# Kernel optimization log

Measured on AMD Instinct MI355X. Metric: run time of the kernel, lower is better.

## Reference

```python
import jax, jax.numpy as jnp
import numpy as np

N = 131072   # total nodes (B*C)
D = 128      # hidden_dim
H = 4        # gat_heads == hgt_heads
HD = 32      # head dim
T = 3        # number of edge types
E = 262144   # edges per edge type
B = 512      # graphs
EPS = 1e-6
SLOPE = 0.2  # LeakyReLU negative slope (module-wide and GAT internal)


def _rmsnorm(x, scale):
    return scale * x * jax.lax.rsqrt(jnp.mean(x * x, axis=-1, keepdims=True) + EPS)


def _gat(x, ei, W, a_src, a_dst, b):
    """HeteroConv(sum) of per-edge-type GATConv (concat heads, self-loops)."""
    loops = jnp.arange(N)

    def one(ei_t, W_t, as_t, ad_t):
        h = (x @ W_t).reshape(N, H, HD)                         # [N,H,HD]
        src = jnp.concatenate([ei_t[0], loops])                 # add self loops
        dst = jnp.concatenate([ei_t[1], loops])
        a = jax.nn.leaky_relu((h * as_t).sum(-1)[src] + (h * ad_t).sum(-1)[dst], SLOPE)  # [E',H]
        m = jax.ops.segment_max(a, dst, num_segments=N)
        ex = jnp.exp(a - m[dst])
        s = jax.ops.segment_sum(ex, dst, num_segments=N)
        alpha = ex / s[dst]                                     # segment softmax per dst
        out = jax.ops.segment_sum(h[src] * alpha[..., None], dst, num_segments=N)
        return out.reshape(N, D)

    return jax.vmap(one)(ei, W, a_src, a_dst).sum(0) + b.sum(0)


def _hgt(x, ei, kw, kb, qw, qb, vw, vb, rel_k, rel_v, rel_p, aw, ab, skip):
    """HGTConv, single node type, T edge types; softmax over all incoming edges."""
    k = (x @ kw + kb).reshape(N, H, HD)
    q = (x @ qw + qb).reshape(N, H, HD)
    v = (x @ vw + vb).reshape(N, H, HD)
    kt = jnp.einsum('nhd,thde->tnhe', k, rel_k)                 # relation-specific keys
    vt = jnp.einsum('nhd,thde->tnhe', v, rel_v)
    k_msg = jax.vmap(lambda a, i: a[i])(kt, ei[:, 0]).reshape(T * E, H, HD)
    v_msg = jax.vmap(lambda a, i: a[i])(vt, ei[:, 0]).reshape(T * E, H, HD)
    dst = ei[:, 1].reshape(T * E)
    p = jnp.broadcast_to(rel_p[:, None, :], (T, E, H)).reshape(T * E, H)
    score = (q[dst] * k_msg).sum(-1) * p / np.sqrt(HD)          # [T*E,H]
    m = jax.ops.segment_max(score, dst, num_segments=N)
    ex = jnp.exp(score - m[dst])
    s = jax.ops.segment_sum(ex, dst, num_segments=N)
    alpha = ex / s[dst]
    out = jax.ops.segment_sum(alpha[..., None] * v_msg, dst, num_segments=N).reshape(N, D)
    out = jax.nn.gelu(out, approximate=False) @ aw + ab
    g = jax.nn.sigmoid(skip)
    return g * out + (1.0 - g) * x


def _res(x_old, x_new, scale):
    # norm -> (dropout is identity in eval) -> residual -> LeakyReLU(0.2)
    return jax.nn.leaky_relu(x_old + _rmsnorm(x_new, scale), SLOPE)


def setup_inputs() -> dict:
    key = jax.random.key(0)
    ks = iter(jax.random.split(key, 48))

    def nrm(shape, std=0.1):
        return jax.random.normal(next(ks), shape, jnp.float32) * std

    inp = {}
    inp['x_cell'] = nrm((N, D), 1.0)
    inp['x_cell_embedded'] = nrm((N, D), 1.0)
    inp['z_h'] = nrm((B, D), 1.0)
    inp['edge_index'] = jax.random.randint(next(ks), (T, 2, E), 0, N)
    for l in ('gat1', 'gat2'):
        inp[l + '_w'] = nrm((T, D, H * HD))
        inp[l + '_att_src'] = nrm((T, H, HD))
        inp[l + '_att_dst'] = nrm((T, H, HD))
        inp[l + '_b'] = jnp.zeros((T, D), jnp.float32)
    inp['norm1_s'] = jnp.ones((D,), jnp.float32)
    inp['norm2_s'] = jnp.ones((D,), jnp.float32)
    inp['norm3_s'] = jnp.ones((D,), jnp.float32)
    for nm in ('k', 'q', 'v'):
        inp['hgt_%s_w' % nm] = nrm((D, D))
        inp['hgt_%s_b' % nm] = jnp.zeros((D,), jnp.float32)
    inp['hgt_rel_k'] = nrm((T, H, HD, HD))
    inp['hgt_rel_v'] = nrm((T, H, HD, HD))
    inp['hgt_rel_p'] = jnp.ones((T, H), jnp.float32)
    inp['hgt_a_w'] = nrm((D, D))
    inp['hgt_a_b'] = jnp.zeros((D,), jnp.float32)
    inp['hgt_skip'] = jnp.ones((), jnp.float32)
    inp['inj_w'] = nrm((D, D))
    inp['inj_b'] = jnp.zeros((D,), jnp.float32)
    inp['film_w1'] = nrm((D, 2 * D))
    inp['film_b1'] = jnp.zeros((2 * D,), jnp.float32)
    inp['film_w2'] = nrm((2 * D, 2 * D), 0.001)
    inp['film_b2'] = jnp.zeros((2 * D,), jnp.float32)
    inp['batch_size'] = B
    return inp


def reference(x_cell, x_cell_embedded, z_h, edge_index,
              gat1_w, gat1_att_src, gat1_att_dst, gat1_b,
              gat2_w, gat2_att_src, gat2_att_dst, gat2_b,
              norm1_s, norm2_s, norm3_s,
              hgt_k_w, hgt_k_b, hgt_q_w, hgt_q_b, hgt_v_w, hgt_v_b,
              hgt_rel_k, hgt_rel_v, hgt_rel_p, hgt_a_w, hgt_a_b, hgt_skip,
              inj_w, inj_b, film_w1, film_b1, film_w2, film_b2, batch_size):
    x1 = _res(x_cell, _gat(x_cell, edge_index, gat1_w, gat1_att_src, gat1_att_dst, gat1_b), norm1_s)
    x2 = _res(x1, _gat(x1, edge_index, gat2_w, gat2_att_src, gat2_att_dst, gat2_b), norm2_s)
    x3 = _res(x2, _hgt(x2, edge_index, hgt_k_w, hgt_k_b, hgt_q_w, hgt_q_b, hgt_v_w, hgt_v_b,
                       hgt_rel_k, hgt_rel_v, hgt_rel_p, hgt_a_w, hgt_a_b, hgt_skip), norm3_s)
    x3 = x3 + x_cell_embedded @ inj_w + inj_b                   # input injection
    # FiLM (per-graph z, fixed batch mode)
    gb = jax.nn.gelu(z_h @ film_w1 + film_b1, approximate=False) @ film_w2 + film_b2
    gamma, beta = jnp.split(gb, 2, axis=-1)
    gamma = 0.1 * jnp.tanh(gamma)
    beta = 0.1 * jnp.tanh(beta)
    C = N // batch_size
    out = (1.0 + gamma)[:, None, :] * x3.reshape(batch_size, C, D) + beta[:, None, :]
    return out.reshape(N, D)
```

## Files before the change

### kernel.cpp

```cpp
#include <hip/hip_runtime.h>
#include <math.h>
#include <cstdint>

#define NN     131072
#define DDIM   128
#define NHEAD  4
#define HDIM   32
#define NTYPE  3
#define NEDGE  262144
#define NGRAPH 512
#define EPSV   1e-6f
#define SLOPEV 0.2f

typedef unsigned short bfraw;
typedef __attribute__((ext_vector_type(8))) short bf16x8;
typedef __attribute__((ext_vector_type(4))) float f32x4;

__device__ __forceinline__ float lrelu(float x){ return x >= 0.f ? x : SLOPEV*x; }
__device__ __forceinline__ float gelu_f(float x){ return 0.5f*x*(1.f+erff(x*0.70710678118654752f)); }
__device__ __forceinline__ bfraw f2bf(float f){
  unsigned int u = __float_as_uint(f);
  u += 0x7fffu + ((u >> 16) & 1u);
  return (bfraw)(u >> 16);
}
__device__ __forceinline__ float4 ld_bf4(const bfraw* p){
  uint2 u = *reinterpret_cast<const uint2*>(p);
  float4 r;
  r.x = __uint_as_float(u.x << 16); r.y = __uint_as_float(u.x & 0xffff0000u);
  r.z = __uint_as_float(u.y << 16); r.w = __uint_as_float(u.y & 0xffff0000u);
  return r;
}
__device__ __forceinline__ bf16x8 pack_bf8(const float* p){
  float4 u = *reinterpret_cast<const float4*>(p);
  float4 v = *reinterpret_cast<const float4*>(p+4);
  bf16x8 r;
  r[0]=(short)f2bf(u.x); r[1]=(short)f2bf(u.y); r[2]=(short)f2bf(u.z); r[3]=(short)f2bf(u.w);
  r[4]=(short)f2bf(v.x); r[5]=(short)f2bf(v.y); r[6]=(short)f2bf(v.z); r[7]=(short)f2bf(v.w);
  return r;
}

__global__ void fill_k(float* __restrict__ p, float v, int n){
  int i = blockIdx.x*blockDim.x + threadIdx.x;
  int stride = gridDim.x*blockDim.x;
  for (; i < n; i += stride) p[i] = v;
}

__global__ void hist_k(const int* __restrict__ ei, int* __restrict__ deg){
  int idx = blockIdx.x*256 + threadIdx.x;
  int t = idx >> 18, e = idx & (NEDGE-1);
  int d = ei[(long)t*2*NEDGE + NEDGE + e];
  atomicAdd(&deg[t*NN + d], 1);
}

__global__ void scan_a_k(const int* __restrict__ deg, int* __restrict__ rp,
                         int* __restrict__ csum){
  __shared__ int sh[256];
  int t = blockIdx.y, chunk = blockIdx.x, tid = threadIdx.x;
  const int* dp = deg + (long)t*NN + chunk*2048 + tid*8;
  int v[8]; int s = 0;
  #pragma unroll
  for (int i=0;i<8;i++){ v[i] = dp[i]; s += v[i]; }
  sh[tid] = s; __syncthreads();
  for (int off=1; off<256; off<<=1){
    int x = (tid>=off) ? sh[tid-off] : 0;
    __syncthreads();
    sh[tid] += x;
    __syncthreads();
  }
  int run = sh[tid] - s;
  int* op = rp + (long)t*(NN+1) + chunk*2048 + tid*8;
  #pragma unroll
  for (int i=0;i<8;i++){ op[i] = run; run += v[i]; }
  if (tid == 255) csum[t*64 + chunk] = sh[255];
}

__global__ void scan_b_k(int* __restrict__ csum){
  __shared__ int sh[64];
  int t = blockIdx.x, tid = threadIdx.x;
  int s = csum[t*64 + tid];
  sh[tid] = s; __syncthreads();
  for (int off=1; off<64; off<<=1){
    int x = (tid>=off) ? sh[tid-off] : 0;
    __syncthreads();
    sh[tid] += x;
    __syncthreads();
  }
  csum[t*64 + tid] = sh[tid] - s;
}

__global__ void scan_c_k(int* __restrict__ rp, const int* __restrict__ csum){
  int t = blockIdx.y, chunk = blockIdx.x, tid = threadIdx.x;
  int add = csum[t*64 + chunk];
  int* op = rp + (long)t*(NN+1) + chunk*2048 + tid*8;
  #pragma unroll
  for (int i=0;i<8;i++) op[i] += add;
  if (chunk == 63 && tid == 255) rp[(long)t*(NN+1) + NN] = NEDGE;
}

__global__ void scatter_k(const int* __restrict__ ei, const int* __restrict__ rp,
                          int* __restrict__ cnt, int* __restrict__ srcs){
  int idx = blockIdx.x*256 + threadIdx.x;
  int t = idx >> 18, e = idx & (NEDGE-1);
  int s = ei[(long)t*2*NEDGE + e];
  int d = ei[(long)t*2*NEDGE + NEDGE + e];
  int pos = rp[(long)t*(NN+1) + d] + atomicAdd(&cnt[t*NN + d], 1);
  srcs[(long)t*NEDGE + pos] = s;
}

__global__ void wswz_k(const float* g0a, const float* g0b, const float* g0c,
                       const float* g1a, const float* g1b, const float* g1c,
                       const float* qw,
                       const float* wk, const float* wv,
                       const float* aw, const float* injw,
                       bfraw* __restrict__ Wall)
{
  int y = blockIdx.y;
  const float* src;
  switch(y){
    case 0: src = g0a; break;  case 1: src = g0b; break;  case 2: src = g0c; break;
    case 3: src = g1a; break;  case 4: src = g1b; break;  case 5: src = g1c; break;
    case 6: src = qw; break;
    case 7: case 8: case 9: src = wk + (long)(y-7)*16384; break;
    case 10: case 11: case 12: src = wv + (long)(y-10)*16384; break;
    case 13: src = aw; break;
    default: src = injw; break;
  }
  int i = blockIdx.x*256 + threadIdx.x;
  int j = i & 7, lane = (i>>3) & 63, kc = (i>>9) & 3, nt = i >> 11;
  int k = kc*32 + ((lane>>4)<<3) + j;
  int n = nt*16 + (lane & 15);
  Wall[(long)y*16384 + i] = f2bf(src[k*DDIM + n]);
}

__global__ void gatproj_k(const float* __restrict__ w, const float* __restrict__ asrc,
                          const float* __restrict__ adst, bfraw* __restrict__ out)
{
  int i = blockIdx.x*256 + threadIdx.x;
  int j = i & 7, lane = (i>>3) & 63, kc = (i>>9) & 3, nt = i >> 11;
  int k = kc*32 + ((lane>>4)<<3) + j;
  int n = nt*16 + (lane & 15);
  float s = 0.f;
  if (n < 24){
    int t = n >> 3, sd = (n >> 2) & 1, hh = n & 3;
    const float* a  = (sd ? adst : asrc) + ((long)t*NHEAD + hh)*HDIM;
    const float* wr = w + ((long)t*DDIM + k)*DDIM + hh*HDIM;
    #pragma unroll 8
    for (int dd=0; dd<HDIM; dd++) s += wr[dd]*a[dd];
  }
  out[i] = f2bf(s);
}

__device__ __forceinline__ void load_afrags_bf16(const bfraw* __restrict__ A,
    long blockRow, int tid, bf16x8 a0[4], bf16x8 a1[4])
{
  const int w = tid >> 6, lane = tid & 63;
  const long rowA = blockRow + w*32 + (lane & 15);
  const bfraw* A0 = A + rowA*DDIM + ((lane>>4)<<3);
  #pragma unroll
  for (int kc=0;kc<4;kc++){
    a0[kc] = *reinterpret_cast<const bf16x8*>(A0 + kc*32);
    a1[kc] = *reinterpret_cast<const bf16x8*>(A0 + 16*DDIM + kc*32);
  }
}

__device__ __forceinline__ void load_afrags_f32(const float* __restrict__ A,
    long blockRow, int tid, bf16x8 a0[4], bf16x8 a1[4])
{
  const int w = tid >> 6, lane = tid & 63;
  const long rowA = blockRow + w*32 + (lane & 15);
  const float* A0 = A + rowA*DDIM + ((lane>>4)<<3);
  #pragma unroll
  for (int kc=0;kc<4;kc++){
    a0[kc] = pack_bf8(A0 + kc*32);
    a1[kc] = pack_bf8(A0 + 16*DDIM + kc*32);
  }
}

__device__ __forceinline__ void mfma_128(const bfraw* Wl, int lane,
    bf16x8 a0[4], bf16x8 a1[4], f32x4 acc0[8], f32x4 acc1[8])
{
  const f32x4 zz = {0.f,0.f,0.f,0.f};
  #pragma unroll
  for (int nt=0;nt<8;nt++){ acc0[nt]=zz; acc1[nt]=zz; }
  #pragma unroll
  for (int nt=0;nt<8;nt++){
    #pragma unroll
    for (int kc=0;kc<4;kc++){
      bf16x8 b = *reinterpret_cast<const bf16x8*>(Wl + ((nt*4+kc)*64 + lane)*8);
      acc0[nt] = __builtin_amdgcn_mfma_f32_16x16x32_bf16(a0[kc], b, acc0[nt], 0, 0, 0);
      acc1[nt] = __builtin_amdgcn_mfma_f32_16x16x32_bf16(a1[kc], b, acc1[nt], 0, 0, 0);
    }
  }
}

__device__ __forceinline__ void gemm_store_bf16(f32x4 acc0[8], f32x4 acc1[8],
    const float* bias, bfraw* __restrict__ Cb, long blockRow, int tid)
{
  const int w = tid>>6, lane = tid&63, q = lane>>4;
  #pragma unroll
  for (int g=0; g<2; g++){
    #pragma unroll
    for (int nt=0;nt<8;nt++){
      int col = nt*16 + (lane & 15);
      float bv = bias ? bias[col] : 0.f;
      #pragma unroll
      for (int r=0;r<4;r++){
        long row = blockRow + w*32 + g*16 + q*4 + r;
        float v = (g ? acc1[nt][r] : acc0[nt][r]) + bv;
        Cb[row*DDIM + col] = f2bf(v);
      }
    }
  }
}

__global__ __launch_bounds__(256) void gemm3_k(
    const bfraw* __restrict__ Ab, const float* __restrict__ Af,
    const bfraw* __restrict__ W0, const bfraw* __restrict__ W1,
    const bfraw* __restrict__ W2,
    const float* __restrict__ b0, const float* __restrict__ b1,
    const float* __restrict__ b2,
    bfraw* __restrict__ O0, bfraw* __restrict__ O1, bfraw* __restrict__ O2,
    const bfraw* __restrict__ Psw, float* __restrict__ SS,
    const bfraw* __restrict__ W3, const float* __restrict__ b3,
    bfraw* __restrict__ O3)
{
  __shared__ bfraw Wl[16384];
  const int tid = threadIdx.x;
  const long blockRow = (long)blockIdx.x * 128;
  const int w = tid >> 6, lane = tid & 63;
  bf16x8 a0[4], a1[4];
  if (Af) load_afrags_f32(Af, blockRow, tid, a0, a1);
  else    load_afrags_bf16(Ab, blockRow, tid, a0, a1);
  const bfraw* Ws[3] = {W0, W1, W2};
  const float* bs[3] = {b0, b1, b2};
  bfraw* Os[3] = {O0, O1, O2};
  #pragma unroll
  for (int t=0;t<3;t++){
    __syncthreads();
    #pragma unroll
    for (int i=0;i<8;i++)
      *reinterpret_cast<uint4*>(Wl + (i*256+tid)*8) =
          *reinterpret_cast<const uint4*>(Ws[t] + (i*256+tid)*8);
    __syncthreads();
    f32x4 acc0[8], acc1[8];
    mfma_128(Wl, lane, a0, a1, acc0, acc1);
    gemm_store_bf16(acc0, acc1, bs[t], Os[t], blockRow, tid);
  }
  if (W3){
    __syncthreads();
    #pragma unroll
    for (int i=0;i<8;i++)
      *reinterpret_cast<uint4*>(Wl + (i*256+tid)*8) =
          *reinterpret_cast<const uint4*>(W3 + (i*256+tid)*8);
    __syncthreads();
    f32x4 acc0[8], acc1[8];
    mfma_128(Wl, lane, a0, a1, acc0, acc1);
    gemm_store_bf16(acc0, acc1, b3, O3, blockRow, tid);
  }
  if (Psw){
    __syncthreads();
    #pragma unroll
    for (int i=0;i<2;i++)
      *reinterpret_cast<uint4*>(Wl + (i*256+tid)*8) =
          *reinterpret_cast<const uint4*>(Psw + (i*256+tid)*8);
    __syncthreads();
    const f32x4 zz = {0.f,0.f,0.f,0.f};
    f32x4 acc0[2], acc1[2];
    #pragma unroll
    for (int nt=0;nt<2;nt++){ acc0[nt]=zz; acc1[nt]=zz; }
    #pragma unroll
    for (int nt=0;nt<2;nt++){
      #pragma unroll
      for (int kc=0;kc<4;kc++){
        bf16x8 b = *reinterpret_cast<const bf16x8*>(Wl + ((nt*4+kc)*64 + lane)*8);
        acc0[nt] = __builtin_amdgcn_mfma_f32_16x16x32_bf16(a0[kc], b, acc0[nt], 0, 0, 0);
        acc1[nt] = __builtin_amdgcn_mfma_f32_16x16x32_bf16(a1[kc], b, acc1[nt], 0, 0, 0);
      }
    }
    const int q = lane >> 4;
    #pragma unroll
    for (int g=0; g<2; g++){
      #pragma unroll
      for (int nt=0;nt<2;nt++){
        int col = nt*16 + (lane & 15);
        if (col < 24){
          int tt = col >> 3, c = col & 7;
          #pragma unroll
          for (int r=0;r<4;r++){
            long row = blockRow + w*32 + g*16 + q*4 + r;
            SS[(((long)tt*NN + row)<<3) + c] = (g ? acc1[nt][r] : acc0[nt][r]);
          }
        }
      }
    }
  }
}

__global__ __launch_bounds__(256) void gemm_r3film_k(
    const bfraw* __restrict__ Aattn, const bfraw* __restrict__ Waw,
    const float* __restrict__ ab, const float* __restrict__ X,
    const float* __restrict__ norm, const float* __restrict__ skip,
    const float* __restrict__ xemb, const bfraw* __restrict__ Winj,
    const float* __restrict__ injb, const float* __restrict__ gbt,
    float* __restrict__ out)
{
  __shared__ bfraw Wl[16384];
  const int tid = threadIdx.x;
  const long blockRow = (long)blockIdx.x * 128;
  #pragma unroll
  for (int i=0;i<8;i++)
    *reinterpret_cast<uint4*>(Wl + (i*256+tid)*8) =
        *reinterpret_cast<const uint4*>(Waw + (i*256+tid)*8);
  __syncthreads();
  bf16x8 a0[4], a1[4];
  load_afrags_bf16(Aattn, blockRow, tid, a0, a1);
  f32x4 accA0[8], accA1[8];
  mfma_128(Wl, tid & 63, a0, a1, accA0, accA1);
  __syncthreads();
  #pragma unroll
  for (int i=0;i<8;i++)
    *reinterpret_cast<uint4*>(Wl + (i*256+tid)*8) =
        *reinterpret_cast<const uint4*>(Winj + (i*256+tid)*8);
  __syncthreads();
  load_afrags_f32(xemb, blockRow, tid, a0, a1);
  f32x4 accB0[8], accB1[8];
  mfma_128(Wl, tid & 63, a0, a1, accB0, accB1);
  const int w = tid>>6, lane = tid&63, q = lane>>4;
  const float gsk = 1.f/(1.f + __expf(-skip[0]));
  #pragma unroll
  for (int g=0; g<2; g++){
    #pragma unroll
    for (int r=0;r<4;r++){
      long row = blockRow + w*32 + g*16 + q*4 + r;
      float vv[8], xx[8];
      float sq = 0.f;
      #pragma unroll
      for (int nt=0;nt<8;nt++){
        int col = nt*16 + (lane & 15);
        float oA = (g ? accA1[nt][r] : accA0[nt][r]) + ab[col];
        float xo = X[row*DDIM + col];
        float v  = gsk*oA + (1.f-gsk)*xo;
        vv[nt] = v; xx[nt] = xo; sq += v*v;
      }
      sq += __shfl_xor(sq, 1, 64);
      sq += __shfl_xor(sq, 2, 64);
      sq += __shfl_xor(sq, 4, 64);
      sq += __shfl_xor(sq, 8, 64);
      float rr = rsqrtf(sq*(1.f/DDIM) + EPSV);
      long gi = row >> 8;
      #pragma unroll
      for (int nt=0;nt<8;nt++){
        int col = nt*16 + (lane & 15);
        float x3 = lrelu(xx[nt] + norm[col]*vv[nt]*rr);
        float vB = (g ? accB1[nt][r] : accB0[nt][r]) + injb[col] + x3;
        out[row*DDIM + col] = (1.f + gbt[gi*256 + col])*vB + gbt[gi*256 + 128 + col];
      }
    }
  }
}

__global__ __launch_bounds__(256) void gat_fused_k(
    const int* __restrict__ rp, const int* __restrict__ srcs,
    const bfraw* __restrict__ H0, const bfraw* __restrict__ H1,
    const bfraw* __restrict__ H2, const float* __restrict__ SS,
    const float* __restrict__ gatb, const float* __restrict__ xold,
    const float* __restrict__ norm, float* __restrict__ X, bfraw* __restrict__ Xb)
{
  int node = blockIdx.x*8 + (threadIdx.x >> 5);
  int l = threadIdx.x & 31;
  int hd = l >> 3;
  const bfraw* Hs[3] = {H0, H1, H2};
  float dsv[3], ssl[3]; float4 hsl[3]; int beg[3], end[3];
  #pragma unroll
  for (int t=0; t<3; t++){
    const float* St = SS + ((long)t*NN)*8;
    dsv[t] = St[(long)node*8 + 4 + hd];
    ssl[t] = St[(long)node*8 + hd];
    hsl[t] = ld_bf4(Hs[t] + (long)node*DDIM + l*4);
    beg[t] = rp[t*(NN+1) + node];
    end[t] = rp[t*(NN+1) + node + 1];
  }
  float tx=0.f, ty=0.f, tz=0.f, tw=0.f;
  #pragma unroll
  for (int t=0; t<3; t++){
    const bfraw* Ht = Hs[t];
    const float* St = SS + ((long)t*NN)*8;
    const int* sp = srcs + (long)t*NEDGE;
    const float d = dsv[t];
    float e = __expf(lrelu(ssl[t] + d));
    float lA = e, lB = 0.f;
    float4 aA = make_float4(e*hsl[t].x, e*hsl[t].y, e*hsl[t].z, e*hsl[t].w);
    float4 aB = make_float4(0.f,0.f,0.f,0.f);
    int p = beg[t];
    for (; p+1 < end[t]; p += 2){
      int s0 = sp[p], s1 = sp[p+1];
      float v0 = St[(long)s0*8 + hd];
      float v1 = St[(long)s1*8 + hd];
      float4 h0 = ld_bf4(Ht + (long)s0*DDIM + l*4);
      float4 h1 = ld_bf4(Ht + (long)s1*DDIM + l*4);
      float e0 = __expf(lrelu(v0 + d));
      float e1 = __expf(lrelu(v1 + d));
      lA += e0; lB += e1;
      aA.x += e0*h0.x; aA.y += e0*h0.y; aA.z += e0*h0.z; aA.w += e0*h0.w;
      aB.x += e1*h1.x; aB.y += e1*h1.y; aB.z += e1*h1.z; aB.w += e1*h1.w;
    }
    if (p < end[t]){
      int s0 = sp[p];
      float e0 = __expf(lrelu(St[(long)s0*8 + hd] + d));
      float4 h0 = ld_bf4(Ht + (long)s0*DDIM + l*4);
      lA += e0;
      aA.x += e0*h0.x; aA.y += e0*h0.y; aA.z += e0*h0.z; aA.w += e0*h0.w;
    }
    float inv = 1.f/(lA + lB);
    tx += (aA.x+aB.x)*inv; ty += (aA.y+aB.y)*inv;
    tz += (aA.z+aB.z)*inv; tw += (aA.w+aB.w)*inv;
  }
  int f = l*4;
  tx += gatb[f]   + gatb[DDIM+f]   + gatb[2*DDIM+f];
  ty += gatb[f+1] + gatb[DDIM+f+1] + gatb[2*DDIM+f+1];
  tz += gatb[f+2] + gatb[DDIM+f+2] + gatb[2*DDIM+f+2];
  tw += gatb[f+3] + gatb[DDIM+f+3] + gatb[2*DDIM+f+3];
  float sq = tx*tx + ty*ty + tz*tz + tw*tw;
  sq += __shfl_xor(sq, 1, 64);
  sq += __shfl_xor(sq, 2, 64);
  sq += __shfl_xor(sq, 4, 64);
  sq += __shfl_xor(sq, 8, 64);
  sq += __shfl_xor(sq, 16, 64);
  float r = rsqrtf(sq*(1.f/DDIM) + EPSV);
  float4 x4 = *reinterpret_cast<const float4*>(xold + (long)node*DDIM + f);
  float4 o;
  o.x = lrelu(x4.x + norm[f]  *tx*r);
  o.y = lrelu(x4.y + norm[f+1]*ty*r);
  o.z = lrelu(x4.z + norm[f+2]*tz*r);
  o.w = lrelu(x4.w + norm[f+3]*tw*r);
  *reinterpret_cast<float4*>(X + (long)node*DDIM + f) = o;
  unsigned int lo = ((unsigned int)f2bf(o.y) << 16) | f2bf(o.x);
  unsigned int hi = ((unsigned int)f2bf(o.w) << 16) | f2bf(o.z);
  *reinterpret_cast<uint2*>(Xb + (long)node*DDIM + f) = make_uint2(lo, hi);
}

__global__ void fold_k(const float* __restrict__ w, const float* __restrict__ b,
                       const float* __restrict__ rel, const float* __restrict__ scl,
                       float* __restrict__ Weff, float* __restrict__ beff)
{
  int idx = blockIdx.x*256 + threadIdx.x;
  if (idx >= NTYPE*DDIM*DDIM) return;
  int he = idx & 127, c = (idx >> 7) & 127, t = idx >> 14;
  int h = he >> 5, e = he & 31;
  float fs = scl ? scl[t*NHEAD + h]*0.17677669529663687f : 1.f;
  const float* wrow = w + (long)c*DDIM + h*HDIM;
  const float* relm = rel + ((long)(t*NHEAD + h)*HDIM)*HDIM + e;
  float s = 0.f;
  #pragma unroll 8
  for (int d=0; d<HDIM; d++) s += wrow[d] * relm[d*HDIM];
  Weff[(long)t*DDIM*DDIM + (long)c*DDIM + he] = s*fs;
  if (c == 0){
    float sb = 0.f;
    #pragma unroll 8
    for (int d=0; d<HDIM; d++) sb += b[h*HDIM+d] * relm[d*HDIM];
    beff[(long)t*DDIM + he] = sb*fs;
  }
}

__global__ __launch_bounds__(256) void hgt_score3_k(
    const int* __restrict__ rp, const int* __restrict__ srcs,
    const bfraw* __restrict__ qb, const bfraw* __restrict__ kt0,
    const bfraw* __restrict__ kt1, const bfraw* __restrict__ kt2,
    float* __restrict__ E)
{
  int node = blockIdx.x*8 + (threadIdx.x >> 5);
  int l = threadIdx.x & 31;
  int hd = l >> 3, sub = l & 7;
  float4 qv = ld_bf4(qb + (long)node*DDIM + l*4);
  const bfraw* kts[3] = {kt0, kt1, kt2};
  #pragma unroll
  for (int t=0; t<3; t++){
    const bfraw* kt = kts[t];
    const int* sp = srcs + (long)t*NEDGE;
    float* Et = E + (long)t*NEDGE*4;
    int beg = rp[t*(NN+1) + node], end = rp[t*(NN+1) + node + 1];
    int p = beg;
    for (; p+1 < end; p += 2){
      int s0 = sp[p], s1 = sp[p+1];
      float4 k0 = ld_bf4(kt + (long)s0*DDIM + l*4);
      float4 k1 = ld_bf4(kt + (long)s1*DDIM + l*4);
      float d0 = qv.x*k0.x + qv.y*k0.y + qv.z*k0.z + qv.w*k0.w;
      float d1 = qv.x*k1.x + qv.y*k1.y + qv.z*k1.z + qv.w*k1.w;
      d0 += __shfl_xor(d0, 1, 64);  d1 += __shfl_xor(d1, 1, 64);
      d0 += __shfl_xor(d0, 2, 64);  d1 += __shfl_xor(d1, 2, 64);
      d0 += __shfl_xor(d0, 4, 64);  d1 += __shfl_xor(d1, 4, 64);
      if (sub == 0){
        Et[(long)p*4 + hd]     = __expf(d0);
        Et[(long)(p+1)*4 + hd] = __expf(d1);
      }
    }
    if (p < end){
      int s0 = sp[p];
      float4 k0 = ld_bf4(kt + (long)s0*DDIM + l*4);
      float d0 = qv.x*k0.x + qv.y*k0.y + qv.z*k0.z + qv.w*k0.w;
      d0 += __shfl_xor(d0, 1, 64);
      d0 += __shfl_xor(d0, 2, 64);
      d0 += __shfl_xor(d0, 4, 64);
      if (sub == 0) Et[(long)p*4 + hd] = __expf(d0);
    }
  }
}

__global__ __launch_bounds__(256) void hgt_acc_fused_k(
    const int* __restrict__ rp, const int* __restrict__ srcs,
    const float* __restrict__ E, const bfraw* __restrict__ V0,
    const bfraw* __restrict__ V1, const bfraw* __restrict__ V2,
    bfraw* __restrict__ out)
{
  int node = blockIdx.x*8 + (threadIdx.x >> 5);
  int l = threadIdx.x & 31;
  int hd = l >> 3;
  float axA=0.f, ayA=0.f, azA=0.f, awA=0.f, lsA=0.f;
  float axB=0.f, ayB=0.f, azB=0.f, awB=0.f, lsB=0.f;
  const bfraw* Vs[3] = {V0, V1, V2};
  #pragma unroll
  for (int t=0; t<3; t++){
    const bfraw* Vt = Vs[t];
    const float* Ep = E + (long)t*NEDGE*4;
    const int* sp = srcs + (long)t*NEDGE;
    int beg = rp[t*(NN+1) + node], end = rp[t*(NN+1) + node + 1];
    int p = beg;
    for (; p+1 < end; p += 2){
      int s0 = sp[p], s1 = sp[p+1];
      float e0 = Ep[(long)p*4 + hd];
      float e1 = Ep[(long)(p+1)*4 + hd];
      float4 v0 = ld_bf4(Vt + (long)s0*DDIM + l*4);
      float4 v1 = ld_bf4(Vt + (long)s1*DDIM + l*4);
      axA += e0*v0.x; ayA += e0*v0.y; azA += e0*v0.z; awA += e0*v0.w; lsA += e0;
      axB += e1*v1.x; ayB += e1*v1.y; azB += e1*v1.z; awB += e1*v1.w; lsB += e1;
    }
    if (p < end){
      int s0 = sp[p];
      float e0 = Ep[(long)p*4 + hd];
      float4 v0 = ld_bf4(Vt + (long)s0*DDIM + l*4);
      axA += e0*v0.x; ayA += e0*v0.y; azA += e0*v0.z; awA += e0*v0.w; lsA += e0;
    }
  }
  float lsum = lsA + lsB;
  float inv = (lsum > 0.f) ? 1.f/lsum : 0.f;
  float o0 = gelu_f((axA+axB)*inv), o1 = gelu_f((ayA+ayB)*inv);
  float o2 = gelu_f((azA+azB)*inv), o3 = gelu_f((awA+awB)*inv);
  unsigned int lo = ((unsigned int)f2bf(o1) << 16) | f2bf(o0);
  unsigned int hi = ((unsigned int)f2bf(o3) << 16) | f2bf(o2);
  *reinterpret_cast<uint2*>(out + (long)node*DDIM + l*4) = make_uint2(lo, hi);
}

__global__ void film1_k(const float* __restrict__ z, const float* __restrict__ w1,
                        const float* __restrict__ b1, float* __restrict__ f1)
{
  int idx = blockIdx.x*256 + threadIdx.x;
  if (idx >= NGRAPH*256) return;
  int j = idx & 255, b = idx >> 8;
  const float* zr = z + (long)b*DDIM;
  float s = b1[j];
  for (int k=0;k<DDIM;k++) s += zr[k] * w1[(long)k*256 + j];
  f1[idx] = gelu_f(s);
}

__global__ void film2_k(const float* __restrict__ f1, const float* __restrict__ w2,
                        const float* __restrict__ b2, float* __restrict__ gb)
{
  int idx = blockIdx.x*256 + threadIdx.x;
  if (idx >= NGRAPH*256) return;
  int j = idx & 255, b = idx >> 8;
  const float* fr = f1 + (long)b*256;
  float s = b2[j];
  for (int k=0;k<256;k++) s += fr[k] * w2[(long)k*256 + j];
  gb[idx] = 0.1f*tanhf(s);
}

extern "C" void kernel_launch(void* const* d_in, const int* in_sizes, int n_in,
                              void* d_out, int out_size, void* d_ws, size_t ws_size,
                              hipStream_t stream)
{
  (void)in_sizes; (void)n_in; (void)out_size; (void)ws_size;
  const float* x_cell = (const float*)d_in[0];
  const float* x_emb  = (const float*)d_in[1];
  const float* z_h    = (const float*)d_in[2];
  const int*   ei     = (const int*)d_in[3];
  const float* gw[2]  = {(const float*)d_in[4],  (const float*)d_in[8]};
  const float* gas[2] = {(const float*)d_in[5],  (const float*)d_in[9]};
  const float* gad[2] = {(const float*)d_in[6],  (const float*)d_in[10]};
  const float* gbi[2] = {(const float*)d_in[7],  (const float*)d_in[11]};
  const float* norm1  = (const float*)d_in[12];
  const float* norm2  = (const float*)d_in[13];
  const float* norm3  = (const float*)d_in[14];
  const float* kw = (const float*)d_in[15]; const float* kb = (const float*)d_in[16];
  const float* qw = (const float*)d_in[17]; const float* qb = (const float*)d_in[18];
  const float* vw = (const float*)d_in[19]; const float* vb = (const float*)d_in[20];
  const float* relk = (const float*)d_in[21];
  const float* relv = (const float*)d_in[22];
  const float* relp = (const float*)d_in[23];
  const float* aw = (const float*)d_in[24]; const float* ab = (const float*)d_in[25];
  const float* skip = (const float*)d_in[26];
  const float* injw = (const float*)d_in[27]; const float* injb = (const float*)d_in[28];
  const float* fw1 = (const float*)d_in[29]; const float* fb1 = (const float*)d_in[30];
  const float* fw2 = (const float*)d_in[31]; const float* fb2 = (const float*)d_in[32];

  const long ND = (long)NN*DDIM;
  float* X    = (float*)d_ws;
  float* K    = X + ND;
  bfraw* Xb   = (bfraw*)(K + ND);
  bfraw* Hb   = Xb + ND;
  float* Sbuf = (float*)(Hb + ND);
  float* sA   = Sbuf + (long)NTYPE*NEDGE*4;
  float* sB   = sA + (long)NN*4;
  float* WkE  = sB + (long)NN*4;
  float* bkE  = WkE + (long)NTYPE*DDIM*DDIM;
  float* WvE  = bkE + (long)NTYPE*DDIM;
  float* bvE  = WvE + (long)NTYPE*DDIM*DDIM;
  bfraw* Pswz = (bfraw*)(bvE + (long)NTYPE*DDIM);
  bfraw* Wall = Pswz + (long)2*4096;
  float* f1b  = (float*)(Wall + (long)15*16384);
  float* gbb  = f1b + (long)NGRAPH*256;
  int*   deg  = (int*)(gbb + (long)NGRAPH*256);
  int*   rp   = deg + (long)NTYPE*NN;
  int*   srcs = rp  + (long)NTYPE*(NN+1);
  int*   csum = srcs + (long)NTYPE*NEDGE;

  bfraw* Kb0 = (bfraw*)K;
  bfraw* Kb1 = Kb0 + ND;
  bfraw* qscr = (bfraw*)d_out;

  const dim3 b256(256);
  float* NF = nullptr;
  bfraw* NB = nullptr; (void)sA; (void)sB;

  fill_k<<<256, b256, 0, stream>>>((float*)deg, 0.f, NTYPE*NN);
  hist_k<<<(NTYPE*NEDGE)/256, b256, 0, stream>>>(ei, deg);
  scan_a_k<<<dim3(64, NTYPE), b256, 0, stream>>>(deg, rp, csum);
  scan_b_k<<<NTYPE, 64, 0, stream>>>(csum);
  scan_c_k<<<dim3(64, NTYPE), b256, 0, stream>>>(rp, csum);
  fill_k<<<256, b256, 0, stream>>>((float*)deg, 0.f, NTYPE*NN);
  scatter_k<<<(NTYPE*NEDGE)/256, b256, 0, stream>>>(ei, rp, deg, srcs);

  fold_k<<<(NTYPE*DDIM*DDIM)/256, b256, 0, stream>>>(kw, kb, relk, relp, WkE, bkE);
  fold_k<<<(NTYPE*DDIM*DDIM)/256, b256, 0, stream>>>(vw, vb, relv, NF, WvE, bvE);
  wswz_k<<<dim3(64, 15), b256, 0, stream>>>(
      gw[0], gw[0]+16384, gw[0]+32768,
      gw[1], gw[1]+16384, gw[1]+32768,
      qw, WkE, WvE, aw, injw, Wall);
  gatproj_k<<<16, b256, 0, stream>>>(gw[0], gas[0], gad[0], Pswz);
  gatproj_k<<<16, b256, 0, stream>>>(gw[1], gas[1], gad[1], Pswz + 4096);

  film1_k<<<(NGRAPH*256)/256, b256, 0, stream>>>(z_h, fw1, fb1, f1b);
  film2_k<<<(NGRAPH*256)/256, b256, 0, stream>>>(f1b, fw2, fb2, gbb);

  for (int layer=0; layer<2; layer++){
    gemm3_k<<<NN/128, b256, 0, stream>>>(
        Xb, (layer==0) ? x_cell : NF,
        Wall + (long)(layer*3+0)*16384, Wall + (long)(layer*3+1)*16384,
        Wall + (long)(layer*3+2)*16384,
        NF, NF, NF,
        Hb, Kb0, Kb1,
        Pswz + (long)layer*4096, Sbuf,
        NB, NF, NB);
    gat_fused_k<<<NN/8, b256, 0, stream>>>(
        rp, srcs, Hb, Kb0, Kb1, Sbuf, gbi[layer],
        (layer==0) ? x_cell : X, (layer==0) ? norm1 : norm2, X, Xb);
  }

  gemm3_k<<<NN/128, b256, 0, stream>>>(
      Xb, NF,
      Wall + (long)7*16384, Wall + (long)8*16384, Wall + (long)9*16384,
      bkE, bkE + DDIM, bkE + 2*DDIM,
      Hb, Kb0, Kb1,
      NB, NF,
      Wall + (long)6*16384, qb, qscr);
  hgt_score3_k<<<NN/8, b256, 0, stream>>>(rp, srcs, qscr, Hb, Kb0, Kb1, Sbuf);
  gemm3_k<<<NN/128, b256, 0, stream>>>(
      Xb, NF,
      Wall + (long)10*16384, Wall + (long)11*16384, Wall + (long)12*16384,
      bvE, bvE + DDIM, bvE + 2*DDIM,
      Hb, Kb0, Kb1,
      NB, NF, NB, NF, NB);
  hgt_acc_fused_k<<<NN/8, b256, 0, stream>>>(rp, srcs, Sbuf, Hb, Kb0, Kb1, Xb);
  gemm_r3film_k<<<NN/128, b256, 0, stream>>>(
      Xb, Wall + (long)13*16384, ab, X, norm3, skip,
      x_emb, Wall + (long)14*16384, injb, gbb, (float*)d_out);
}
```

Before: 869.8 us.

## Fuse weight prep kernels, vectorize edge CSR build, widen GAT per-lane work

Merges the fold, swizzle and GAT projection prep kernels into a single launch that swizzles the folded K/V weights directly. It also drops the second counter-clear fill by zeroing counters inside scan_c. The histogram and scatter kernels now process two edges per thread using int2 loads. The GAT aggregation kernel maps 16 lanes per node with 8 features each using 128-bit bf16 loads, which halves the thread count and uses a shorter shuffle reduction, at the cost of more registers per thread.

```diff
diff --git a/kernel.cpp b/kernel.cpp
--- a/kernel.cpp
+++ b/kernel.cpp
@@ -30,6 +30,15 @@
   r.z = __uint_as_float(u.y << 16); r.w = __uint_as_float(u.y & 0xffff0000u);
   return r;
 }
+__device__ __forceinline__ void ld_bf8(const bfraw* p, float* o){
+  uint4 v = *reinterpret_cast<const uint4*>(p);
+  unsigned int w[4] = {v.x, v.y, v.z, v.w};
+  #pragma unroll
+  for (int i=0;i<4;i++){
+    o[2*i]   = __uint_as_float(w[i] << 16);
+    o[2*i+1] = __uint_as_float(w[i] & 0xffff0000u);
+  }
+}
 __device__ __forceinline__ bf16x8 pack_bf8(const float* p){
   float4 u = *reinterpret_cast<const float4*>(p);
   float4 v = *reinterpret_cast<const float4*>(p+4);
@@ -47,9 +56,10 @@
 
 __global__ void hist_k(const int* __restrict__ ei, int* __restrict__ deg){
   int idx = blockIdx.x*256 + threadIdx.x;
-  int t = idx >> 18, e = idx & (NEDGE-1);
-  int d = ei[(long)t*2*NEDGE + NEDGE + e];
-  atomicAdd(&deg[t*NN + d], 1);
+  int t = idx >> 17, e = (idx & 131071)*2;
+  int2 d = *reinterpret_cast<const int2*>(ei + (long)t*2*NEDGE + NEDGE + e);
+  atomicAdd(&deg[t*NN + d.x], 1);
+  atomicAdd(&deg[t*NN + d.y], 1);
 }
 
 __global__ void scan_a_k(const int* __restrict__ deg, int* __restrict__ rp,
@@ -88,66 +98,89 @@
   csum[t*64 + tid] = sh[tid] - s;
 }
 
-__global__ void scan_c_k(int* __restrict__ rp, const int* __restrict__ csum){
+__global__ void scan_c_k(int* __restrict__ rp, const int* __restrict__ csum,
+                         int* __restrict__ cnt){
   int t = blockIdx.y, chunk = blockIdx.x, tid = threadIdx.x;
   int add = csum[t*64 + chunk];
   int* op = rp + (long)t*(NN+1) + chunk*2048 + tid*8;
-  #pragma unroll
-  for (int i=0;i<8;i++) op[i] += add;
+  int* cp = cnt + (long)t*NN + chunk*2048 + tid*8;
+  #pragma unroll
+  for (int i=0;i<8;i++){ op[i] += add; cp[i] = 0; }
   if (chunk == 63 && tid == 255) rp[(long)t*(NN+1) + NN] = NEDGE;
 }
 
 __global__ void scatter_k(const int* __restrict__ ei, const int* __restrict__ rp,
                           int* __restrict__ cnt, int* __restrict__ srcs){
   int idx = blockIdx.x*256 + threadIdx.x;
-  int t = idx >> 18, e = idx & (NEDGE-1);
-  int s = ei[(long)t*2*NEDGE + e];
-  int d = ei[(long)t*2*NEDGE + NEDGE + e];
-  int pos = rp[(long)t*(NN+1) + d] + atomicAdd(&cnt[t*NN + d], 1);
-  srcs[(long)t*NEDGE + pos] = s;
-}
-
-__global__ void wswz_k(const float* g0a, const float* g0b, const float* g0c,
-                       const float* g1a, const float* g1b, const float* g1c,
-                       const float* qw,
-                       const float* wk, const float* wv,
-                       const float* aw, const float* injw,
-                       bfraw* __restrict__ Wall)
+  int t = idx >> 17, e = (idx & 131071)*2;
+  int2 s = *reinterpret_cast<const int2*>(ei + (long)t*2*NEDGE + e);
+  int2 d = *reinterpret_cast<const int2*>(ei + (long)t*2*NEDGE + NEDGE + e);
+  int p0 = rp[(long)t*(NN+1) + d.x] + atomicAdd(&cnt[t*NN + d.x], 1);
+  srcs[(long)t*NEDGE + p0] = s.x;
+  int p1 = rp[(long)t*(NN+1) + d.y] + atomicAdd(&cnt[t*NN + d.y], 1);
+  srcs[(long)t*NEDGE + p1] = s.y;
+}
+
+__global__ void wswz_all_k(
+    const float* g0a, const float* g0b, const float* g0c,
+    const float* g1a, const float* g1b, const float* g1c,
+    const float* qw, const float* aw, const float* injw,
+    const float* kw, const float* kb, const float* relk, const float* relp,
+    const float* vw, const float* vb, const float* relv,
+    const float* gw0, const float* gas0, const float* gad0,
+    const float* gw1, const float* gas1, const float* gad1,
+    bfraw* __restrict__ Wall, bfraw* __restrict__ Pswz,
+    float* __restrict__ bkE, float* __restrict__ bvE)
 {
   int y = blockIdx.y;
-  const float* src;
-  switch(y){
-    case 0: src = g0a; break;  case 1: src = g0b; break;  case 2: src = g0c; break;
-    case 3: src = g1a; break;  case 4: src = g1b; break;  case 5: src = g1c; break;
-    case 6: src = qw; break;
-    case 7: case 8: case 9: src = wk + (long)(y-7)*16384; break;
-    case 10: case 11: case 12: src = wv + (long)(y-10)*16384; break;
-    case 13: src = aw; break;
-    default: src = injw; break;
-  }
   int i = blockIdx.x*256 + threadIdx.x;
   int j = i & 7, lane = (i>>3) & 63, kc = (i>>9) & 3, nt = i >> 11;
   int k = kc*32 + ((lane>>4)<<3) + j;
   int n = nt*16 + (lane & 15);
-  Wall[(long)y*16384 + i] = f2bf(src[k*DDIM + n]);
-}
-
-__global__ void gatproj_k(const float* __restrict__ w, const float* __restrict__ asrc,
-                          const float* __restrict__ adst, bfraw* __restrict__ out)
-{
-  int i = blockIdx.x*256 + threadIdx.x;
-  int j = i & 7, lane = (i>>3) & 63, kc = (i>>9) & 3, nt = i >> 11;
-  int k = kc*32 + ((lane>>4)<<3) + j;
-  int n = nt*16 + (lane & 15);
-  float s = 0.f;
-  if (n < 24){
-    int t = n >> 3, sd = (n >> 2) & 1, hh = n & 3;
-    const float* a  = (sd ? adst : asrc) + ((long)t*NHEAD + hh)*HDIM;
-    const float* wr = w + ((long)t*DDIM + k)*DDIM + hh*HDIM;
+  if (y < 7 || y == 13 || y == 14){
+    const float* src;
+    switch(y){
+      case 0: src = g0a; break;  case 1: src = g0b; break;  case 2: src = g0c; break;
+      case 3: src = g1a; break;  case 4: src = g1b; break;  case 5: src = g1c; break;
+      case 6: src = qw; break;   case 13: src = aw; break;  default: src = injw; break;
+    }
+    Wall[(long)y*16384 + i] = f2bf(src[k*DDIM + n]);
+  } else if (y < 13){
+    int isK = (y < 10);
+    int t = isK ? (y-7) : (y-10);
+    const float* w   = isK ? kw : vw;
+    const float* b   = isK ? kb : vb;
+    const float* rel = isK ? relk : relv;
+    int h = n >> 5, e = n & 31;
+    float fs = isK ? relp[t*NHEAD + h]*0.17677669529663687f : 1.f;
+    const float* wrow = w + (long)k*DDIM + h*HDIM;
+    const float* relm = rel + ((long)(t*NHEAD + h)*HDIM)*HDIM + e;
+    float s = 0.f;
     #pragma unroll 8
-    for (int dd=0; dd<HDIM; dd++) s += wr[dd]*a[dd];
-  }
-  out[i] = f2bf(s);
+    for (int dd=0; dd<HDIM; dd++) s += wrow[dd] * relm[dd*HDIM];
+    Wall[(long)y*16384 + i] = f2bf(s*fs);
+    if (k == 0){
+      float sb = 0.f;
+      #pragma unroll 8
+      for (int dd=0; dd<HDIM; dd++) sb += b[h*HDIM+dd] * relm[dd*HDIM];
+      (isK ? bkE : bvE)[t*DDIM + n] = sb*fs;
+    }
+  } else {
+    if (blockIdx.x >= 16) return;
+    int layer = y - 15;
+    const float* w   = layer ? gw1 : gw0;
+    const float* as_ = layer ? gas1 : gas0;
+    const float* ad_ = layer ? gad1 : gad0;
+    float s = 0.f;
+    if (n < 24){
+      int t = n >> 3, sd = (n >> 2) & 1, hh = n & 3;
+      const float* a  = (sd ? ad_ : as_) + ((long)t*NHEAD + hh)*HDIM;
+      const float* wr = w + ((long)t*DDIM + k)*DDIM + hh*HDIM;
+      #pragma unroll 8
+      for (int dd=0; dd<HDIM; dd++) s += wr[dd]*a[dd];
+    }
+    Pswz[(long)layer*4096 + i] = f2bf(s);
+  }
 }
 
 __device__ __forceinline__ void load_afrags_bf16(const bfraw* __restrict__ A,
@@ -366,100 +399,93 @@
     const float* __restrict__ gatb, const float* __restrict__ xold,
     const float* __restrict__ norm, float* __restrict__ X, bfraw* __restrict__ Xb)
 {
-  int node = blockIdx.x*8 + (threadIdx.x >> 5);
-  int l = threadIdx.x & 31;
-  int hd = l >> 3;
+  int node = blockIdx.x*16 + (threadIdx.x >> 4);
+  int l = threadIdx.x & 15;
+  int hd = l >> 2;
   const bfraw* Hs[3] = {H0, H1, H2};
-  float dsv[3], ssl[3]; float4 hsl[3]; int beg[3], end[3];
+  float dsv[3], ssl[3]; int beg[3], end[3];
   #pragma unroll
   for (int t=0; t<3; t++){
     const float* St = SS + ((long)t*NN)*8;
     dsv[t] = St[(long)node*8 + 4 + hd];
     ssl[t] = St[(long)node*8 + hd];
-    hsl[t] = ld_bf4(Hs[t] + (long)node*DDIM + l*4);
     beg[t] = rp[t*(NN+1) + node];
     end[t] = rp[t*(NN+1) + node + 1];
   }
-  float tx=0.f, ty=0.f, tz=0.f, tw=0.f;
+  float tx[8];
+  #pragma unroll
+  for (int j=0;j<8;j++) tx[j] = 0.f;
   #pragma unroll
   for (int t=0; t<3; t++){
     const bfraw* Ht = Hs[t];
     const float* St = SS + ((long)t*NN)*8;
     const int* sp = srcs + (long)t*NEDGE;
     const float d = dsv[t];
+    float hs[8];
+    ld_bf8(Ht + (long)node*DDIM + l*8, hs);
     float e = __expf(lrelu(ssl[t] + d));
     float lA = e, lB = 0.f;
-    float4 aA = make_float4(e*hsl[t].x, e*hsl[t].y, e*hsl[t].z, e*hsl[t].w);
-    float4 aB = make_float4(0.f,0.f,0.f,0.f);
+    float aA[8], aB[8];
+    #pragma unroll
+    for (int j=0;j<8;j++){ aA[j] = e*hs[j]; aB[j] = 0.f; }
     int p = beg[t];
     for (; p+1 < end[t]; p += 2){
       int s0 = sp[p], s1 = sp[p+1];
       float v0 = St[(long)s0*8 + hd];
       float v1 = St[(long)s1*8 + hd];
-      float4 h0 = ld_bf4(Ht + (long)s0*DDIM + l*4);
-      float4 h1 = ld_bf4(Ht + (long)s1*DDIM + l*4);
+      float h0[8], h1[8];
+      ld_bf8(Ht + (long)s0*DDIM + l*8, h0);
+      ld_bf8(Ht + (long)s1*DDIM + l*8, h1);
       float e0 = __expf(lrelu(v0 + d));
       float e1 = __expf(lrelu(v1 + d));
       lA += e0; lB += e1;
-      aA.x += e0*h0.x; aA.y += e0*h0.y; aA.z += e0*h0.z; aA.w += e0*h0.w;
-      aB.x += e1*h1.x; aB.y += e1*h1.y; aB.z += e1*h1.z; aB.w += e1*h1.w;
+      #pragma unroll
+      for (int j=0;j<8;j++){ aA[j] += e0*h0[j]; aB[j] += e1*h1[j]; }
     }
     if (p < end[t]){
       int s0 = sp[p];
       float e0 = __expf(lrelu(St[(long)s0*8 + hd] + d));
-      float4 h0 = ld_bf4(Ht + (long)s0*DDIM + l*4);
+      float h0[8];
+      ld_bf8(Ht + (long)s0*DDIM + l*8, h0);
       lA += e0;
-      aA.x += e0*h0.x; aA.y += e0*h0.y; aA.z += e0*h0.z; aA.w += e0*h0.w;
+      #pragma unroll
+      for (int j=0;j<8;j++) aA[j] += e0*h0[j];
     }
     float inv = 1.f/(lA + lB);
-    tx += (aA.x+aB.x)*inv; ty += (aA.y+aB.y)*inv;
-    tz += (aA.z+aB.z)*inv; tw += (aA.w+aB.w)*inv;
-  }
-  int f = l*4;
-  tx += gatb[f]   + gatb[DDIM+f]   + gatb[2*DDIM+f];
-  ty += gatb[f+1] + gatb[DDIM+f+1] + gatb[2*DDIM+f+1];
-  tz += gatb[f+2] + gatb[DDIM+f+2] + gatb[2*DDIM+f+2];
-  tw += gatb[f+3] + gatb[DDIM+f+3] + gatb[2*DDIM+f+3];
-  float sq = tx*tx + ty*ty + tz*tz + tw*tw;
+    #pragma unroll
+    for (int j=0;j<8;j++) tx[j] += (aA[j] + aB[j])*inv;
+  }
+  int f = l*8;
+  #pragma unroll
+  for (int j=0;j<8;j++)
+    tx[j] += gatb[f+j] + gatb[DDIM+f+j] + gatb[2*DDIM+f+j];
+  float sq = 0.f;
+  #pragma unroll
+  for (int j=0;j<8;j++) sq += tx[j]*tx[j];
   sq += __shfl_xor(sq, 1, 64);
   sq += __shfl_xor(sq, 2, 64);
   sq += __shfl_xor(sq, 4, 64);
   sq += __shfl_xor(sq, 8, 64);
-  sq += __shfl_xor(sq, 16, 64);
   float r = rsqrtf(sq*(1.f/DDIM) + EPSV);
-  float4 x4 = *reinterpret_cast<const float4*>(xold + (long)node*DDIM + f);
-  float4 o;
-  o.x = lrelu(x4.x + norm[f]  *tx*r);
-  o.y = lrelu(x4.y + norm[f+1]*ty*r);
-  o.z = lrelu(x4.z + norm[f+2]*tz*r);
-  o.w = lrelu(x4.w + norm[f+3]*tw*r);
-  *reinterpret_cast<float4*>(X + (long)node*DDIM + f) = o;
-  unsigned int lo = ((unsigned int)f2bf(o.y) << 16) | f2bf(o.x);
-  unsigned int hi = ((unsigned int)f2bf(o.w) << 16) | f2bf(o.z);
-  *reinterpret_cast<uint2*>(Xb + (long)node*DDIM + f) = make_uint2(lo, hi);
-}
-
-__global__ void fold_k(const float* __restrict__ w, const float* __restrict__ b,
-                       const float* __restrict__ rel, const float* __restrict__ scl,
-                       float* __restrict__ Weff, float* __restrict__ beff)
-{
-  int idx = blockIdx.x*256 + threadIdx.x;
-  if (idx >= NTYPE*DDIM*DDIM) return;
-  int he = idx & 127, c = (idx >> 7) & 127, t = idx >> 14;
-  int h = he >> 5, e = he & 31;
-  float fs = scl ? scl[t*NHEAD + h]*0.17677669529663687f : 1.f;
-  const float* wrow = w + (long)c*DDIM + h*HDIM;
-  const float* relm = rel + ((long)(t*NHEAD + h)*HDIM)*HDIM + e;
-  float s = 0.f;
-  #pragma unroll 8
-  for (int d=0; d<HDIM; d++) s += wrow[d] * relm[d*HDIM];
-  Weff[(long)t*DDIM*DDIM + (long)c*DDIM + he] = s*fs;
-  if (c == 0){
-    float sb = 0.f;
-    #pragma unroll 8
-    for (int d=0; d<HDIM; d++) sb += b[h*HDIM+d] * relm[d*HDIM];
-    beff[(long)t*DDIM + he] = sb*fs;
-  }
+  float4 xa = *reinterpret_cast<const float4*>(xold + (long)node*DDIM + f);
+  float4 xb = *reinterpret_cast<const float4*>(xold + (long)node*DDIM + f + 4);
+  float o[8];
+  o[0] = lrelu(xa.x + norm[f+0]*tx[0]*r);
+  o[1] = lrelu(xa.y + norm[f+1]*tx[1]*r);
+  o[2] = lrelu(xa.z + norm[f+2]*tx[2]*r);
+  o[3] = lrelu(xa.w + norm[f+3]*tx[3]*r);
+  o[4] = lrelu(xb.x + norm[f+4]*tx[4]*r);
+  o[5] = lrelu(xb.y + norm[f+5]*tx[5]*r);
+  o[6] = lrelu(xb.z + norm[f+6]*tx[6]*r);
+  o[7] = lrelu(xb.w + norm[f+7]*tx[7]*r);
+  *reinterpret_cast<float4*>(X + (long)node*DDIM + f)     = make_float4(o[0],o[1],o[2],o[3]);
+  *reinterpret_cast<float4*>(X + (long)node*DDIM + f + 4) = make_float4(o[4],o[5],o[6],o[7]);
+  uint4 u;
+  u.x = ((unsigned int)f2bf(o[1]) << 16) | f2bf(o[0]);
+  u.y = ((unsigned int)f2bf(o[3]) << 16) | f2bf(o[2]);
+  u.z = ((unsigned int)f2bf(o[5]) << 16) | f2bf(o[4]);
+  u.w = ((unsigned int)f2bf(o[7]) << 16) | f2bf(o[6]);
+  *reinterpret_cast<uint4*>(Xb + (long)node*DDIM + f) = u;
 }
 
 __global__ __launch_bounds__(256) void hgt_score3_k(
@@ -629,24 +655,22 @@
 
   const dim3 b256(256);
   float* NF = nullptr;
-  bfraw* NB = nullptr; (void)sA; (void)sB;
+  bfraw* NB = nullptr; (void)sA; (void)sB; (void)WkE; (void)WvE;
 
   fill_k<<<256, b256, 0, stream>>>((float*)deg, 0.f, NTYPE*NN);
-  hist_k<<<(NTYPE*NEDGE)/256, b256, 0, stream>>>(ei, deg);
+  hist_k<<<(NTYPE*NEDGE/2)/256, b256, 0, stream>>>(ei, deg);
   scan_a_k<<<dim3(64, NTYPE), b256, 0, stream>>>(deg, rp, csum);
   scan_b_k<<<NTYPE, 64, 0, stream>>>(csum);
-  scan_c_k<<<dim3(64, NTYPE), b256, 0, stream>>>(rp, csum);
-  fill_k<<<256, b256, 0, stream>>>((float*)deg, 0.f, NTYPE*NN);
-  scatter_k<<<(NTYPE*NEDGE)/256, b256, 0, stream>>>(ei, rp, deg, srcs);
-
-  fold_k<<<(NTYPE*DDIM*DDIM)/256, b256, 0, stream>>>(kw, kb, relk, relp, WkE, bkE);
-  fold_k<<<(NTYPE*DDIM*DDIM)/256, b256, 0, stream>>>(vw, vb, relv, NF, WvE, bvE);
-  wswz_k<<<dim3(64, 15), b256, 0, stream>>>(
+  scan_c_k<<<dim3(64, NTYPE), b256, 0, stream>>>(rp, csum, deg);
+  scatter_k<<<(NTYPE*NEDGE/2)/256, b256, 0, stream>>>(ei, rp, deg, srcs);
+
+  wswz_all_k<<<dim3(64, 17), b256, 0, stream>>>(
       gw[0], gw[0]+16384, gw[0]+32768,
       gw[1], gw[1]+16384, gw[1]+32768,
-      qw, WkE, WvE, aw, injw, Wall);
-  gatproj_k<<<16, b256, 0, stream>>>(gw[0], gas[0], gad[0], Pswz);
-  gatproj_k<<<16, b256, 0, stream>>>(gw[1], gas[1], gad[1], Pswz + 4096);
+      qw, aw, injw,
+      kw, kb, relk, relp, vw, vb, relv,
+      gw[0], gas[0], gad[0], gw[1], gas[1], gad[1],
+      Wall, Pswz, bkE, bvE);
 
   film1_k<<<(NGRAPH*256)/256, b256, 0, stream>>>(z_h, fw1, fb1, f1b);
   film2_k<<<(NGRAPH*256)/256, b256, 0, stream>>>(f1b, fw2, fb2, gbb);
@@ -660,7 +684,7 @@
         Hb, Kb0, Kb1,
         Pswz + (long)layer*4096, Sbuf,
         NB, NF, NB);
-    gat_fused_k<<<NN/8, b256, 0, stream>>>(
+    gat_fused_k<<<NN/16, b256, 0, stream>>>(
         rp, srcs, Hb, Kb0, Kb1, Sbuf, gbi[layer],
         (layer==0) ? x_cell : X, (layer==0) ? norm1 : norm2, X, Xb);
   }
```

Measured after the change: 848.9 us. 2.4% less time.
